# Kernel tuning notes

Hardware: AMD Instinct MI355X
Metric: run time of the kernel (lower is better)

## Reference

```python
import jax, jax.numpy as jnp
import numpy as np

N_NODES = 100000


def gcn_conv(x, edge_index, W, b):
    """PyG GCNConv: symmetric normalization with added self-loops.
    x: [N, Fin], edge_index: [2, E], W: [Fin, Fout], b: [Fout]
    """
    n = x.shape[0]
    h = x @ W  # [N, Fout] dense transform first (standard GCNConv order)
    loops = jnp.arange(n, dtype=edge_index.dtype)
    src = jnp.concatenate([edge_index[0], loops])  # self-loops appended
    dst = jnp.concatenate([edge_index[1], loops])
    deg = jax.ops.segment_sum(jnp.ones_like(dst, dtype=h.dtype), dst, num_segments=n)
    dinv = jax.lax.rsqrt(deg)  # deg >= 1 thanks to self-loops
    norm = dinv[src] * dinv[dst]  # [E+N]
    msgs = h[src] * norm[:, None]  # gather + scale
    out = jax.ops.segment_sum(msgs, dst, num_segments=n)  # scatter-add
    return out + b


def setup_inputs() -> dict:
    key = jax.random.key(0)
    k = jax.random.split(key, 9)
    in_c, hid, out_c = 128, 128, 64
    n_edges = 1600000
    x = jax.random.normal(k[0], (N_NODES, in_c), dtype=jnp.float32)
    edge_index = jax.random.randint(k[1], (2, n_edges), 0, N_NODES, dtype=jnp.int64)
    def lin(kw, kb, fan_in, fan_out):
        bound = 1.0 / np.sqrt(fan_in)
        W = jax.random.uniform(kw, (fan_in, fan_out), jnp.float32, -bound, bound)
        b = jax.random.uniform(kb, (fan_out,), jnp.float32, -bound, bound)
        return W, b
    W1, b1 = lin(k[2], k[3], in_c, hid)
    W2, b2 = lin(k[4], k[5], hid, hid)
    Wf, bf = lin(k[6], k[7], hid, out_c)
    return {"x": x, "edge_index": edge_index, "W1": W1, "b1": b1,
            "W2": W2, "b2": b2, "Wf": Wf, "bf": bf}


def reference(x, edge_index, W1, b1, W2, b2, Wf, bf):
    h = jax.nn.relu(gcn_conv(x, edge_index, W1, b1))
    h = jax.nn.relu(gcn_conv(h, edge_index, W2, b2))
    return h @ Wf + bf
```

## Files before the change

kernel.cpp:

```cpp
#include <hip/hip_runtime.h>
#include <stdint.h>

typedef short short8 __attribute__((ext_vector_type(8)));
typedef float floatx4 __attribute__((ext_vector_type(4)));
typedef float f32x2 __attribute__((ext_vector_type(2)));

#define BK 256

static __device__ __forceinline__ float bflo(unsigned int u) {
    union { unsigned int i; float f; } v; v.i = u << 16; return v.f;
}
static __device__ __forceinline__ float bfhi(unsigned int u) {
    union { unsigned int i; float f; } v; v.i = u & 0xffff0000u; return v.f;
}
static __device__ __forceinline__ unsigned short f2bf(float f) {
    union { float f; unsigned int i; } v; v.f = f;
    unsigned int u = v.i;
    unsigned int r = u + 0x7fffu + ((u >> 16) & 1u);
    return (unsigned short)(r >> 16);
}
static __device__ __forceinline__ f32x2 unp2(unsigned int u) {
    union { unsigned int i; float f; } lo, hi;
    lo.i = u << 16; hi.i = u & 0xffff0000u;
    f32x2 r; r.x = lo.f; r.y = hi.f; return r;
}


__global__ void k_zero_cnt(int* bucket_cnt, int K) {
    int i = blockIdx.x * 256 + threadIdx.x;
    if (i < K) bucket_cnt[i] = 0;
}

__global__ __launch_bounds__(256) void k_hist(const int* __restrict__ dst, int* bucket_cnt,
                                              int E, int N, int K) {
    __shared__ int h[4][512];
    int t = threadIdx.x, w = t >> 6;
    for (int i = t; i < 4 * 512; i += 256) ((int*)h)[i] = 0;
    __syncthreads();
    int per = (E + gridDim.x - 1) / gridDim.x;
    int lo = blockIdx.x * per, hi = min(lo + per, E);
    for (int e = lo + t; e < hi; e += 256) {
        unsigned int d = (unsigned int)dst[e];
        if (d < (unsigned int)N) atomicAdd(&h[w][d >> 8], 1);
    }
    __syncthreads();
    for (int i = t; i < K; i += 256) {
        int c = h[0][i] + h[1][i] + h[2][i] + h[3][i];
        if (c) atomicAdd(&bucket_cnt[i], c);
    }
}

__global__ void k_scanK(const int* __restrict__ bucket_cnt, int* bucket_off, int* bucket_cur,
                        int* row_start, int K, int N) {
    __shared__ int s[512];
    int t = threadIdx.x;
    int v = (t < K) ? bucket_cnt[t] : 0;
    s[t] = v; __syncthreads();
    for (int off = 1; off < 512; off <<= 1) {
        int x = (t >= off) ? s[t - off] : 0;
        __syncthreads();
        s[t] += x;
        __syncthreads();
    }
    if (t < K) { bucket_off[t] = s[t] - v; bucket_cur[t] = s[t] - v; }
    if (t == K - 1) { bucket_off[K] = s[t]; row_start[N] = s[t]; }
}

__global__ __launch_bounds__(256) void k_binscatter(const int* __restrict__ src,
                                                    const int* __restrict__ dst,
                                                    int* bucket_cur, unsigned int* __restrict__ tmp,
                                                    int E, int N, int K) {
    __shared__ int h[4][512];
    int t = threadIdx.x, w = t >> 6;
    for (int i = t; i < 4 * 512; i += 256) ((int*)h)[i] = 0;
    __syncthreads();
    int per = (E + gridDim.x - 1) / gridDim.x;
    int lo = blockIdx.x * per, hi = min(lo + per, E);
    for (int e = lo + t; e < hi; e += 256) {
        unsigned int d = (unsigned int)dst[e];
        if (d < (unsigned int)N) atomicAdd(&h[w][d >> 8], 1);
    }
    __syncthreads();
    for (int k = t; k < K; k += 256) {
        int c0 = h[0][k], c1 = h[1][k], c2 = h[2][k], c3 = h[3][k];
        int tot = c0 + c1 + c2 + c3;
        int base = tot ? atomicAdd(&bucket_cur[k], tot) : 0;
        h[0][k] = base; h[1][k] = base + c0; h[2][k] = base + c0 + c1;
        h[3][k] = base + c0 + c1 + c2;
    }
    __syncthreads();
    for (int e = lo + t; e < hi; e += 256) {
        unsigned int d = (unsigned int)dst[e];
        if (d < (unsigned int)N) {
            unsigned int sv = (unsigned int)src[e];
            if (sv >= (unsigned int)N) sv = 0;
            int p = atomicAdd(&h[w][d >> 8], 1);
            tmp[p] = (sv << 8) | (d & 255u);
        }
    }
}

__global__ __launch_bounds__(256) void k_fine(const unsigned int* __restrict__ tmp,
                                              const int* __restrict__ bucket_off,
                                              int* __restrict__ row_start, float* __restrict__ dinv,
                                              int* __restrict__ csr, int N) {
    __shared__ int deg4[4][BK];
    __shared__ int scn[BK];
    __shared__ int cur[BK];
    int b = blockIdx.x, t = threadIdx.x, w = t >> 6;
    int lo = bucket_off[b], hi = bucket_off[b + 1];
    for (int i = t; i < 4 * BK; i += 256) ((int*)deg4)[i] = 0;
    __syncthreads();
    for (int e = lo + t; e < hi; e += 256) atomicAdd(&deg4[w][tmp[e] & 255u], 1);
    __syncthreads();
    int v = deg4[0][t] + deg4[1][t] + deg4[2][t] + deg4[3][t];
    scn[t] = v; __syncthreads();
    for (int off = 1; off < 256; off <<= 1) {
        int x = (t >= off) ? scn[t - off] : 0;
        __syncthreads();
        scn[t] += x;
        __syncthreads();
    }
    int rs = lo + scn[t] - v;
    cur[t] = rs;
    int node = b * BK + t;
    if (node < N) { row_start[node] = rs; dinv[node] = rsqrtf((float)(v + 1)); }
    __syncthreads();
    for (int e = lo + t; e < hi; e += 256) {
        unsigned int p = tmp[e];
        int pos = atomicAdd(&cur[p & 255u], 1);
        csr[pos] = (int)(p >> 8);
    }
}


__global__ void k_wconv_all(const float* __restrict__ W1, const float* __restrict__ W2,
                            const float* __restrict__ Wf, unsigned short* __restrict__ wb1,
                            unsigned short* __restrict__ wb2, unsigned short* __restrict__ wbf) {
    int i = blockIdx.x * 256 + threadIdx.x;
    if (i < 16384) {
        int k = i >> 7, n = i & 127;
        wb1[n * 128 + k] = f2bf(W1[i]);
    } else if (i < 32768) {
        int j = i - 16384, k = j >> 7, n = j & 127;
        wb2[n * 128 + k] = f2bf(W2[j]);
    } else if (i < 40960) {
        int j = i - 32768, k = j >> 6, n = j & 63;
        wbf[n * 128 + k] = f2bf(Wf[j]);
    }
}


template <int NOUT, bool SCALE, bool BIAS, bool XF32, bool OUTF32>
__global__ __launch_bounds__(256, 2) void k_gemm(
    const void* __restrict__ Xv, const unsigned short* __restrict__ Wbf,
    const float* __restrict__ bias, const float* __restrict__ dinv,
    void* __restrict__ outv, int M, int MB) {
    __shared__ __align__(16) unsigned short Wl[NOUT * 136];
    int t = threadIdx.x;
    for (int c = t; c < NOUT * 16; c += 256) {
        short8 v = *(const short8*)(Wbf + (size_t)c * 8);
        *(short8*)(&Wl[(c >> 4) * 136 + (c & 15) * 8]) = v;
    }
    __syncthreads();

    int wave = t >> 6, lane = t & 63;
    int quad = lane >> 4, l16 = lane & 15;
    constexpr int NT = NOUT / 16;

    for (int mb = blockIdx.x; mb < MB; mb += gridDim.x) {
        int m0 = mb * 64 + wave * 16;
        int mr = m0 + l16;
        int mrc = mr < M ? mr : M - 1;

        floatx4 acc[NT];
#pragma unroll
        for (int i = 0; i < NT; i++) acc[i] = (floatx4){0.f, 0.f, 0.f, 0.f};

#pragma unroll
        for (int kc = 0; kc < 4; kc++) {
            short8 a;
            if (XF32) {
                const float* X = (const float*)Xv;
                const float* p = X + (size_t)mrc * 128 + kc * 32 + quad * 8;
                float4 xa = *(const float4*)p;
                float4 xb = *(const float4*)(p + 4);
                a[0] = (short)f2bf(xa.x); a[1] = (short)f2bf(xa.y);
                a[2] = (short)f2bf(xa.z); a[3] = (short)f2bf(xa.w);
                a[4] = (short)f2bf(xb.x); a[5] = (short)f2bf(xb.y);
                a[6] = (short)f2bf(xb.z); a[7] = (short)f2bf(xb.w);
            } else {
                const unsigned short* X = (const unsigned short*)Xv;
                a = *(const short8*)(X + (size_t)mrc * 128 + kc * 32 + quad * 8);
            }
#pragma unroll
            for (int nt = 0; nt < NT; nt++) {
                short8 b = *(const short8*)(&Wl[(nt * 16 + l16) * 136 + kc * 32 + quad * 8]);
                acc[nt] = __builtin_amdgcn_mfma_f32_16x16x32_bf16(a, b, acc[nt], 0, 0, 0);
            }
        }

#pragma unroll
        for (int i = 0; i < 4; i++) {
            int r = m0 + quad * 4 + i;
            if (r >= M) continue;
            float sc = SCALE ? dinv[r] : 1.0f;
#pragma unroll
            for (int nt = 0; nt < NT; nt++) {
                int n = nt * 16 + l16;
                float v = acc[nt][i] * sc;
                if (BIAS) v += bias[n];
                if (OUTF32) {
                    ((float*)outv)[(size_t)r * NOUT + n] = v;
                } else {
                    ((unsigned short*)outv)[(size_t)r * NOUT + n] = f2bf(v);
                }
            }
        }
    }
}


__global__ __launch_bounds__(256, 8) void k_aggregate(
    const unsigned short* __restrict__ Hs, const int* __restrict__ csr,
    const int* __restrict__ row_start,
    const float* __restrict__ dinv, const float* __restrict__ bias,
    unsigned short* __restrict__ out, int N, int E) {
    int wave = threadIdx.x >> 6, lane = threadIdx.x & 63;
    int half = lane >> 5;
    int grp = (lane >> 4) & 1;
    int c16 = lane & 15;
    int l32 = lane & 31;
    int sbase = half << 5;
    int node = blockIdx.x * 8 + wave * 2 + half;
    int Nm1 = N - 1;
    int node_c = node < N ? node : Nm1;
    unsigned int cb2 = (unsigned int)c16 << 4;
    const char* Hb = (const char*)Hs;

    int start = row_start[node_c];
    int end = row_start[node_c + 1];
    if (start < 0) start = 0;
    if (end > E) end = E;
    int cnt = end - start;
    if (cnt < 0) cnt = 0;

    uint4 us = *(const uint4*)(Hb + (((size_t)node_c << 8) | cb2));

    int pre = cnt < 32 ? cnt : 32;
    int idxv = 0;
    if (l32 < pre) idxv = min(max(csr[start + l32], 0), Nm1);

    f32x2 a01 = {0.f, 0.f}, a23 = {0.f, 0.f}, a45 = {0.f, 0.f}, a67 = {0.f, 0.f};
#define ACC8(u) do { a01 += unp2((u).x); a23 += unp2((u).y); \
                     a45 += unp2((u).z); a67 += unp2((u).w); } while (0)

    int full2 = pre >> 1;
    int it = 0;
    for (; it + 4 <= full2; it += 4) {
        int p = it * 2 + grp;
        int i0 = __shfl(idxv, sbase + p);
        int i1 = __shfl(idxv, sbase + p + 2);
        int i2 = __shfl(idxv, sbase + p + 4);
        int i3 = __shfl(idxv, sbase + p + 6);
        uint4 u0 = *(const uint4*)(Hb + (((unsigned int)i0 << 8) | cb2));
        uint4 u1 = *(const uint4*)(Hb + (((unsigned int)i1 << 8) | cb2));
        uint4 u2 = *(const uint4*)(Hb + (((unsigned int)i2 << 8) | cb2));
        uint4 u3 = *(const uint4*)(Hb + (((unsigned int)i3 << 8) | cb2));
        ACC8(u0); ACC8(u1); ACC8(u2); ACC8(u3);
    }
    for (; it < full2; it++) {
        int i0 = __shfl(idxv, sbase + it * 2 + grp);
        uint4 u0 = *(const uint4*)(Hb + (((unsigned int)i0 << 8) | cb2));
        ACC8(u0);
    }
    int eT = full2 * 2 + grp;
    int iT = __shfl(idxv, sbase + (eT < pre ? eT : 0));
    if (eT < pre) {
        uint4 u0 = *(const uint4*)(Hb + (((unsigned int)iT << 8) | cb2));
        ACC8(u0);
    }
    for (int e = start + 32 + grp; e < end; e += 2) {
        int ii = min(max(csr[e], 0), Nm1);
        uint4 u = *(const uint4*)(Hb + (((unsigned int)ii << 8) | cb2));
        ACC8(u);
    }
#undef ACC8

    float a0 = a01.x, a1 = a01.y, a2 = a23.x, a3 = a23.y;
    float a4 = a45.x, a5 = a45.y, a6 = a67.x, a7 = a67.y;

    a0 += __shfl_xor(a0, 16); a1 += __shfl_xor(a1, 16); a2 += __shfl_xor(a2, 16);
    a3 += __shfl_xor(a3, 16); a4 += __shfl_xor(a4, 16); a5 += __shfl_xor(a5, 16);
    a6 += __shfl_xor(a6, 16); a7 += __shfl_xor(a7, 16);

    a0 += bflo(us.x); a1 += bfhi(us.x); a2 += bflo(us.y); a3 += bfhi(us.y);
    a4 += bflo(us.z); a5 += bfhi(us.z); a6 += bflo(us.w); a7 += bfhi(us.w);

    float di = dinv[node_c];
    float4 b0 = *(const float4*)(bias + c16 * 8);
    float4 b1 = *(const float4*)(bias + c16 * 8 + 4);
    float r0 = fmaxf(fmaf(di, a0, b0.x), 0.f);
    float r1 = fmaxf(fmaf(di, a1, b0.y), 0.f);
    float r2 = fmaxf(fmaf(di, a2, b0.z), 0.f);
    float r3 = fmaxf(fmaf(di, a3, b0.w), 0.f);
    float r4 = fmaxf(fmaf(di, a4, b1.x), 0.f);
    float r5 = fmaxf(fmaf(di, a5, b1.y), 0.f);
    float r6 = fmaxf(fmaf(di, a6, b1.z), 0.f);
    float r7 = fmaxf(fmaf(di, a7, b1.w), 0.f);
    if (grp == 0 && node < N) {
        uint4 o;
        o.x = (unsigned int)f2bf(r0) | ((unsigned int)f2bf(r1) << 16);
        o.y = (unsigned int)f2bf(r2) | ((unsigned int)f2bf(r3) << 16);
        o.z = (unsigned int)f2bf(r4) | ((unsigned int)f2bf(r5) << 16);
        o.w = (unsigned int)f2bf(r6) | ((unsigned int)f2bf(r7) << 16);
        *(uint4*)(out + (((size_t)node << 7) | (size_t)(c16 * 8))) = o;
    }
}


extern "C" void kernel_launch(void* const* d_in, const int* in_sizes, int n_in,
                              void* d_out, int out_size, void* d_ws, size_t ws_size,
                              hipStream_t stream) {
    const float* x  = (const float*)d_in[0];
    const int* ei   = (const int*)d_in[1];
    const float* W1 = (const float*)d_in[2];
    const float* b1 = (const float*)d_in[3];
    const float* W2 = (const float*)d_in[4];
    const float* b2 = (const float*)d_in[5];
    const float* Wf = (const float*)d_in[6];
    const float* bf = (const float*)d_in[7];

    int N = in_sizes[0] / 128;
    int E = in_sizes[1] / 2;
    const int* src = ei;
    const int* dst = ei + E;
    int K = (N + BK - 1) / BK;
    if (N >= (1 << 24) || K > 512) return;

    size_t need = 0;
    auto pad = [](size_t b) { return (b + 255) & ~(size_t)255; };
    size_t o_bcnt = need; need += pad(512 * 4);
    size_t o_boff = need; need += pad(513 * 4);
    size_t o_bcur = need; need += pad(512 * 4);
    size_t o_rs   = need; need += pad(((size_t)N + 1) * 4);
    size_t o_dinv = need; need += pad((size_t)N * 4);
    size_t o_wbf  = need; need += pad((16384 + 16384 + 8192) * 2);
    size_t o_csr  = need; need += pad((size_t)E * 4);
    size_t o_hs   = need; need += pad((size_t)N * 128 * 2);
    size_t o_a    = need; need += pad((size_t)N * 128 * 2);
    if (ws_size < need) return;
    if ((size_t)E * 4 > (size_t)N * 128 * 2) return;

    char* ws = (char*)d_ws;
    int* bucket_cnt = (int*)(ws + o_bcnt);
    int* bucket_off = (int*)(ws + o_boff);
    int* bucket_cur = (int*)(ws + o_bcur);
    int* row_start  = (int*)(ws + o_rs);
    float* dinv     = (float*)(ws + o_dinv);
    unsigned short* wb1 = (unsigned short*)(ws + o_wbf);
    unsigned short* wb2 = wb1 + 16384;
    unsigned short* wbf = wb2 + 16384;
    int* csr        = (int*)(ws + o_csr);
    unsigned short* Hs = (unsigned short*)(ws + o_hs);
    unsigned short* A  = (unsigned short*)(ws + o_a);
    unsigned int* tmp  = (unsigned int*)A;

    k_wconv_all<<<160, 256, 0, stream>>>(W1, W2, Wf, wb1, wb2, wbf);

    k_zero_cnt<<<2, 256, 0, stream>>>(bucket_cnt, 512);
    k_hist<<<256, 256, 0, stream>>>(dst, bucket_cnt, E, N, K);
    k_scanK<<<1, 512, 0, stream>>>(bucket_cnt, bucket_off, bucket_cur, row_start, K, N);
    k_binscatter<<<256, 256, 0, stream>>>(src, dst, bucket_cur, tmp, E, N, K);
    k_fine<<<K, 256, 0, stream>>>(tmp, bucket_off, row_start, dinv, csr, N);

    int MB = (N + 63) / 64;
    int GG = (MB + 1) / 2;

    k_gemm<128, true, false, true, false><<<GG, 256, 0, stream>>>(x, wb1, nullptr, dinv, Hs, N, MB);
    k_aggregate<<<(N + 7) / 8, 256, 0, stream>>>(Hs, csr, row_start, dinv, b1, A, N, E);
    k_gemm<128, true, false, false, false><<<GG, 256, 0, stream>>>(A, wb2, nullptr, dinv, Hs, N, MB);
    k_aggregate<<<(N + 7) / 8, 256, 0, stream>>>(Hs, csr, row_start, dinv, b2, A, N, E);
    k_gemm<64, false, true, false, true><<<GG, 256, 0, stream>>>(A, wbf, bf, nullptr, d_out, N, MB);
}
```

Before: 327.6 us.

## Fuse CSR construction kernels into one cooperative kernel with grid syncs

Replaces the six preprocessing launches (weight conversion, counter zeroing, histogram, bucket scan, bin scatter, fine sort) with a single cooperative kernel that separates the phases with grid-wide syncs. The histogram is recomputed per block in the scatter phase so each block can reserve contiguous slots per bucket. This is meant to remove launch gaps and per-kernel tail effects. It adds grid.sync costs, requires every block to be co-resident, and falls back to the old launch sequence if the cooperative launch fails.

```diff
diff --git a/kernel.cpp b/kernel.cpp
--- a/kernel.cpp
+++ b/kernel.cpp
@@ -1,4 +1,5 @@
 #include <hip/hip_runtime.h>
+#include <hip/hip_cooperative_groups.h>
 #include <stdint.h>
 
 typedef short short8 __attribute__((ext_vector_type(8)));
@@ -23,6 +24,137 @@
     union { unsigned int i; float f; } lo, hi;
     lo.i = u << 16; hi.i = u & 0xffff0000u;
     f32x2 r; r.x = lo.f; r.y = hi.f; return r;
+}
+
+
+static __device__ void wconv_body(int i, const float* W1, const float* W2, const float* Wf,
+                                  unsigned short* wb1, unsigned short* wb2, unsigned short* wbf) {
+    if (i < 16384) {
+        int k = i >> 7, n = i & 127;
+        wb1[n * 128 + k] = f2bf(W1[i]);
+    } else if (i < 32768) {
+        int j = i - 16384, k = j >> 7, n = j & 127;
+        wb2[n * 128 + k] = f2bf(W2[j]);
+    } else if (i < 40960) {
+        int j = i - 32768, k = j >> 6, n = j & 63;
+        wbf[n * 128 + k] = f2bf(Wf[j]);
+    }
+}
+
+
+__global__ __launch_bounds__(256) void k_csr_fused(
+    const int* __restrict__ src, const int* __restrict__ dst,
+    const float* __restrict__ W1, const float* __restrict__ W2, const float* __restrict__ Wf,
+    unsigned short* __restrict__ wb1, unsigned short* __restrict__ wb2,
+    unsigned short* __restrict__ wbf,
+    int* bucket_cnt, int* bucket_off, int* bucket_cur,
+    int* __restrict__ row_start, float* __restrict__ dinv,
+    unsigned int* __restrict__ tmp, int* __restrict__ csr,
+    int E, int N, int K) {
+    cooperative_groups::grid_group grid = cooperative_groups::this_grid();
+    __shared__ int h[4][512];
+    __shared__ int s[512];
+    __shared__ int deg4[4][BK];
+    int t = threadIdx.x, w = t >> 6;
+    int G = gridDim.x;
+    int g0 = blockIdx.x * 256 + t, gs = G * 256;
+
+    for (int i = g0; i < 512; i += gs) bucket_cnt[i] = 0;
+    for (int i = g0; i < 40960; i += gs) wconv_body(i, W1, W2, Wf, wb1, wb2, wbf);
+    grid.sync();
+
+    {
+        for (int i = t; i < 4 * 512; i += 256) ((int*)h)[i] = 0;
+        __syncthreads();
+        int per = (E + G - 1) / G;
+        int lo = blockIdx.x * per, hi = min(lo + per, E);
+        for (int e = lo + t; e < hi; e += 256) {
+            unsigned int d = (unsigned int)dst[e];
+            if (d < (unsigned int)N) atomicAdd(&h[w][d >> 8], 1);
+        }
+        __syncthreads();
+        for (int i = t; i < K; i += 256) {
+            int c = h[0][i] + h[1][i] + h[2][i] + h[3][i];
+            if (c) atomicAdd(&bucket_cnt[i], c);
+        }
+    }
+    grid.sync();
+
+    if (blockIdx.x == 0) {
+        int e0 = bucket_cnt[2 * t], e1 = bucket_cnt[2 * t + 1];
+        int p = e0 + e1;
+        s[t] = p; __syncthreads();
+        for (int off = 1; off < 256; off <<= 1) {
+            int x = (t >= off) ? s[t - off] : 0;
+            __syncthreads();
+            s[t] += x;
+            __syncthreads();
+        }
+        int incl = s[t];
+        int excl = incl - p;
+        bucket_off[2 * t] = excl;        bucket_cur[2 * t] = excl;
+        bucket_off[2 * t + 1] = excl + e0; bucket_cur[2 * t + 1] = excl + e0;
+        if (t == 255) { bucket_off[512] = incl; row_start[N] = incl; }
+    }
+    grid.sync();
+
+    {
+        for (int i = t; i < 4 * 512; i += 256) ((int*)h)[i] = 0;
+        __syncthreads();
+        int per = (E + G - 1) / G;
+        int lo = blockIdx.x * per, hi = min(lo + per, E);
+        for (int e = lo + t; e < hi; e += 256) {
+            unsigned int d = (unsigned int)dst[e];
+            if (d < (unsigned int)N) atomicAdd(&h[w][d >> 8], 1);
+        }
+        __syncthreads();
+        for (int k = t; k < K; k += 256) {
+            int c0 = h[0][k], c1 = h[1][k], c2 = h[2][k], c3 = h[3][k];
+            int tot = c0 + c1 + c2 + c3;
+            int base = tot ? atomicAdd(&bucket_cur[k], tot) : 0;
+            h[0][k] = base; h[1][k] = base + c0; h[2][k] = base + c0 + c1;
+            h[3][k] = base + c0 + c1 + c2;
+        }
+        __syncthreads();
+        for (int e = lo + t; e < hi; e += 256) {
+            unsigned int d = (unsigned int)dst[e];
+            if (d < (unsigned int)N) {
+                unsigned int sv = (unsigned int)src[e];
+                if (sv >= (unsigned int)N) sv = 0;
+                int p = atomicAdd(&h[w][d >> 8], 1);
+                tmp[p] = (sv << 8) | (d & 255u);
+            }
+        }
+    }
+    grid.sync();
+
+    int* scn = s;
+    int* cur = s + 256;
+    for (int b = blockIdx.x; b < K; b += G) {
+        int lo = bucket_off[b], hi = bucket_off[b + 1];
+        for (int i = t; i < 4 * BK; i += 256) ((int*)deg4)[i] = 0;
+        __syncthreads();
+        for (int e = lo + t; e < hi; e += 256) atomicAdd(&deg4[w][tmp[e] & 255u], 1);
+        __syncthreads();
+        int v = deg4[0][t] + deg4[1][t] + deg4[2][t] + deg4[3][t];
+        scn[t] = v; __syncthreads();
+        for (int off = 1; off < 256; off <<= 1) {
+            int x = (t >= off) ? scn[t - off] : 0;
+            __syncthreads();
+            scn[t] += x;
+            __syncthreads();
+        }
+        int rs = lo + scn[t] - v;
+        cur[t] = rs;
+        int node = b * BK + t;
+        if (node < N) { row_start[node] = rs; dinv[node] = rsqrtf((float)(v + 1)); }
+        __syncthreads();
+        for (int e = lo + t; e < hi; e += 256) {
+            unsigned int p = tmp[e];
+            int pos = atomicAdd(&cur[p & 255u], 1);
+            csr[pos] = (int)(p >> 8);
+        }
+    }
 }
 
 
@@ -133,21 +265,11 @@
     }
 }
 
-
 __global__ void k_wconv_all(const float* __restrict__ W1, const float* __restrict__ W2,
                             const float* __restrict__ Wf, unsigned short* __restrict__ wb1,
                             unsigned short* __restrict__ wb2, unsigned short* __restrict__ wbf) {
     int i = blockIdx.x * 256 + threadIdx.x;
-    if (i < 16384) {
-        int k = i >> 7, n = i & 127;
-        wb1[n * 128 + k] = f2bf(W1[i]);
-    } else if (i < 32768) {
-        int j = i - 16384, k = j >> 7, n = j & 127;
-        wb2[n * 128 + k] = f2bf(W2[j]);
-    } else if (i < 40960) {
-        int j = i - 32768, k = j >> 6, n = j & 63;
-        wbf[n * 128 + k] = f2bf(Wf[j]);
-    }
+    wconv_body(i, W1, W2, Wf, wb1, wb2, wbf);
 }
 
 
@@ -366,13 +488,31 @@
     unsigned short* A  = (unsigned short*)(ws + o_a);
     unsigned int* tmp  = (unsigned int*)A;
 
-    k_wconv_all<<<160, 256, 0, stream>>>(W1, W2, Wf, wb1, wb2, wbf);
-
-    k_zero_cnt<<<2, 256, 0, stream>>>(bucket_cnt, 512);
-    k_hist<<<256, 256, 0, stream>>>(dst, bucket_cnt, E, N, K);
-    k_scanK<<<1, 512, 0, stream>>>(bucket_cnt, bucket_off, bucket_cur, row_start, K, N);
-    k_binscatter<<<256, 256, 0, stream>>>(src, dst, bucket_cur, tmp, E, N, K);
-    k_fine<<<K, 256, 0, stream>>>(tmp, bucket_off, row_start, dinv, csr, N);
+    int G = K > 256 ? K : 256;
+    {
+        const int* srcp = src; const int* dstp = dst;
+        const float *W1p = W1, *W2p = W2, *Wfp = Wf;
+        unsigned short *wb1p = wb1, *wb2p = wb2, *wbfp = wbf;
+        int Ev = E, Nv = N, Kv = K;
+        void* args[] = {
+            (void*)&srcp, (void*)&dstp,
+            (void*)&W1p, (void*)&W2p, (void*)&Wfp,
+            (void*)&wb1p, (void*)&wb2p, (void*)&wbfp,
+            (void*)&bucket_cnt, (void*)&bucket_off, (void*)&bucket_cur,
+            (void*)&row_start, (void*)&dinv,
+            (void*)&tmp, (void*)&csr,
+            (void*)&Ev, (void*)&Nv, (void*)&Kv};
+        hipError_t ce = hipLaunchCooperativeKernel((const void*)k_csr_fused,
+                                                   dim3(G), dim3(256), args, 0, stream);
+        if (ce != hipSuccess) {
+            k_wconv_all<<<160, 256, 0, stream>>>(W1, W2, Wf, wb1, wb2, wbf);
+            k_zero_cnt<<<2, 256, 0, stream>>>(bucket_cnt, 512);
+            k_hist<<<256, 256, 0, stream>>>(dst, bucket_cnt, E, N, K);
+            k_scanK<<<1, 512, 0, stream>>>(bucket_cnt, bucket_off, bucket_cur, row_start, K, N);
+            k_binscatter<<<256, 256, 0, stream>>>(src, dst, bucket_cur, tmp, E, N, K);
+            k_fine<<<K, 256, 0, stream>>>(tmp, bucket_off, row_start, dinv, csr, N);
+        }
+    }
 
     int MB = (N + 63) / 64;
     int GG = (MB + 1) / 2;
```

After: 520.0 us. 58.7% more time.

## Fuse neighbor aggregation with following GEMM via shared-memory tile

Applied to the files above, without the earlier changes.

Merges each aggregation kernel with the next dense transform. Each block aggregates 64 nodes into an LDS tile, then runs bf16 MFMA against the weights, so the intermediate activation no longer makes a round trip through global memory and two launches are removed. It also folds the bucket-counter zeroing into the weight-conversion kernel. In exchange, occupancy drops from 8 to 3 blocks per CU, and each wave handles 8 nodes serially, which reduces the latency hiding available to the irregular gathers.

```diff
diff --git a/kernel.cpp b/kernel.cpp
--- a/kernel.cpp
+++ b/kernel.cpp
@@ -26,9 +26,22 @@
 }
 
 
-__global__ void k_zero_cnt(int* bucket_cnt, int K) {
+__global__ void k_wconv_all(const float* __restrict__ W1, const float* __restrict__ W2,
+                            const float* __restrict__ Wf, unsigned short* __restrict__ wb1,
+                            unsigned short* __restrict__ wb2, unsigned short* __restrict__ wbf,
+                            int* __restrict__ bucket_cnt) {
     int i = blockIdx.x * 256 + threadIdx.x;
-    if (i < K) bucket_cnt[i] = 0;
+    if (i < 512) bucket_cnt[i] = 0;
+    if (i < 16384) {
+        int k = i >> 7, n = i & 127;
+        wb1[n * 128 + k] = f2bf(W1[i]);
+    } else if (i < 32768) {
+        int j = i - 16384, k = j >> 7, n = j & 127;
+        wb2[n * 128 + k] = f2bf(W2[j]);
+    } else if (i < 40960) {
+        int j = i - 32768, k = j >> 6, n = j & 63;
+        wbf[n * 128 + k] = f2bf(Wf[j]);
+    }
 }
 
 __global__ __launch_bounds__(256) void k_hist(const int* __restrict__ dst, int* bucket_cnt,
@@ -130,23 +143,6 @@
         unsigned int p = tmp[e];
         int pos = atomicAdd(&cur[p & 255u], 1);
         csr[pos] = (int)(p >> 8);
-    }
-}
-
-
-__global__ void k_wconv_all(const float* __restrict__ W1, const float* __restrict__ W2,
-                            const float* __restrict__ Wf, unsigned short* __restrict__ wb1,
-                            unsigned short* __restrict__ wb2, unsigned short* __restrict__ wbf) {
-    int i = blockIdx.x * 256 + threadIdx.x;
-    if (i < 16384) {
-        int k = i >> 7, n = i & 127;
-        wb1[n * 128 + k] = f2bf(W1[i]);
-    } else if (i < 32768) {
-        int j = i - 16384, k = j >> 7, n = j & 127;
-        wb2[n * 128 + k] = f2bf(W2[j]);
-    } else if (i < 40960) {
-        int j = i - 32768, k = j >> 6, n = j & 63;
-        wbf[n * 128 + k] = f2bf(Wf[j]);
     }
 }
 
@@ -221,100 +217,147 @@
 }
 
 
-__global__ __launch_bounds__(256, 8) void k_aggregate(
+template <int NOUT, bool SCALE, bool BIAS, bool OUTF32>
+__global__ __launch_bounds__(256, 3) void k_agg_gemm(
     const unsigned short* __restrict__ Hs, const int* __restrict__ csr,
-    const int* __restrict__ row_start,
-    const float* __restrict__ dinv, const float* __restrict__ bias,
-    unsigned short* __restrict__ out, int N, int E) {
-    int wave = threadIdx.x >> 6, lane = threadIdx.x & 63;
+    const int* __restrict__ row_start, const float* __restrict__ dinv,
+    const float* __restrict__ bias_agg, const unsigned short* __restrict__ Wbf,
+    const float* __restrict__ bias_out, void* __restrict__ outv,
+    int N, int E) {
+    __shared__ __align__(16) unsigned short Wl[NOUT * 136];
+    __shared__ __align__(16) unsigned short Xl[64 * 136];
+    int t = threadIdx.x;
+    for (int c = t; c < NOUT * 16; c += 256) {
+        short8 v = *(const short8*)(Wbf + (size_t)c * 8);
+        *(short8*)(&Wl[(c >> 4) * 136 + (c & 15) * 8]) = v;
+    }
+
+    int wave = t >> 6, lane = t & 63;
     int half = lane >> 5;
     int grp = (lane >> 4) & 1;
     int c16 = lane & 15;
     int l32 = lane & 31;
     int sbase = half << 5;
-    int node = blockIdx.x * 8 + wave * 2 + half;
     int Nm1 = N - 1;
-    int node_c = node < N ? node : Nm1;
     unsigned int cb2 = (unsigned int)c16 << 4;
     const char* Hb = (const char*)Hs;
 
-    int start = row_start[node_c];
-    int end = row_start[node_c + 1];
-    if (start < 0) start = 0;
-    if (end > E) end = E;
-    int cnt = end - start;
-    if (cnt < 0) cnt = 0;
-
-    uint4 us = *(const uint4*)(Hb + (((size_t)node_c << 8) | cb2));
-
-    int pre = cnt < 32 ? cnt : 32;
-    int idxv = 0;
-    if (l32 < pre) idxv = min(max(csr[start + l32], 0), Nm1);
-
-    f32x2 a01 = {0.f, 0.f}, a23 = {0.f, 0.f}, a45 = {0.f, 0.f}, a67 = {0.f, 0.f};
+    float4 bA0 = *(const float4*)(bias_agg + c16 * 8);
+    float4 bA1 = *(const float4*)(bias_agg + c16 * 8 + 4);
+
+    for (int j = 0; j < 8; ++j) {
+        int lr = wave * 16 + 2 * j + half;
+        int node = blockIdx.x * 64 + lr;
+        int node_c = node < N ? node : Nm1;
+
+        int start = row_start[node_c];
+        int end = row_start[node_c + 1];
+        if (start < 0) start = 0;
+        if (end > E) end = E;
+        int cnt = end - start;
+        if (cnt < 0) cnt = 0;
+
+        uint4 us = *(const uint4*)(Hb + (((size_t)node_c << 8) | cb2));
+
+        int pre = cnt < 32 ? cnt : 32;
+        int idxv = 0;
+        if (l32 < pre) idxv = min(max(csr[start + l32], 0), Nm1);
+
+        f32x2 a01 = {0.f, 0.f}, a23 = {0.f, 0.f}, a45 = {0.f, 0.f}, a67 = {0.f, 0.f};
 #define ACC8(u) do { a01 += unp2((u).x); a23 += unp2((u).y); \
                      a45 += unp2((u).z); a67 += unp2((u).w); } while (0)
-
-    int full2 = pre >> 1;
-    int it = 0;
-    for (; it + 4 <= full2; it += 4) {
-        int p = it * 2 + grp;
-        int i0 = __shfl(idxv, sbase + p);
-        int i1 = __shfl(idxv, sbase + p + 2);
-        int i2 = __shfl(idxv, sbase + p + 4);
-        int i3 = __shfl(idxv, sbase + p + 6);
-        uint4 u0 = *(const uint4*)(Hb + (((unsigned int)i0 << 8) | cb2));
-        uint4 u1 = *(const uint4*)(Hb + (((unsigned int)i1 << 8) | cb2));
-        uint4 u2 = *(const uint4*)(Hb + (((unsigned int)i2 << 8) | cb2));
-        uint4 u3 = *(const uint4*)(Hb + (((unsigned int)i3 << 8) | cb2));
-        ACC8(u0); ACC8(u1); ACC8(u2); ACC8(u3);
-    }
-    for (; it < full2; it++) {
-        int i0 = __shfl(idxv, sbase + it * 2 + grp);
-        uint4 u0 = *(const uint4*)(Hb + (((unsigned int)i0 << 8) | cb2));
-        ACC8(u0);
-    }
-    int eT = full2 * 2 + grp;
-    int iT = __shfl(idxv, sbase + (eT < pre ? eT : 0));
-    if (eT < pre) {
-        uint4 u0 = *(const uint4*)(Hb + (((unsigned int)iT << 8) | cb2));
-        ACC8(u0);
-    }
-    for (int e = start + 32 + grp; e < end; e += 2) {
-        int ii = min(max(csr[e], 0), Nm1);
-        uint4 u = *(const uint4*)(Hb + (((unsigned int)ii << 8) | cb2));
-        ACC8(u);
-    }
+        int full2 = pre >> 1;
+        int it = 0;
+        for (; it + 4 <= full2; it += 4) {
+            int p = it * 2 + grp;
+            int i0 = __shfl(idxv, sbase + p);
+            int i1 = __shfl(idxv, sbase + p + 2);
+            int i2 = __shfl(idxv, sbase + p + 4);
+            int i3 = __shfl(idxv, sbase + p + 6);
+            uint4 u0 = *(const uint4*)(Hb + (((unsigned int)i0 << 8) | cb2));
+            uint4 u1 = *(const uint4*)(Hb + (((unsigned int)i1 << 8) | cb2));
+            uint4 u2 = *(const uint4*)(Hb + (((unsigned int)i2 << 8) | cb2));
+            uint4 u3 = *(const uint4*)(Hb + (((unsigned int)i3 << 8) | cb2));
+            ACC8(u0); ACC8(u1); ACC8(u2); ACC8(u3);
+        }
+        for (; it < full2; it++) {
+            int i0 = __shfl(idxv, sbase + it * 2 + grp);
+            uint4 u0 = *(const uint4*)(Hb + (((unsigned int)i0 << 8) | cb2));
+            ACC8(u0);
+        }
+        int eT = full2 * 2 + grp;
+        int iT = __shfl(idxv, sbase + (eT < pre ? eT : 0));
+        if (eT < pre) {
+            uint4 u0 = *(const uint4*)(Hb + (((unsigned int)iT << 8) | cb2));
+            ACC8(u0);
+        }
+        for (int e = start + 32 + grp; e < end; e += 2) {
+            int ii = min(max(csr[e], 0), Nm1);
+            uint4 u = *(const uint4*)(Hb + (((unsigned int)ii << 8) | cb2));
+            ACC8(u);
+        }
 #undef ACC8
 
-    float a0 = a01.x, a1 = a01.y, a2 = a23.x, a3 = a23.y;
-    float a4 = a45.x, a5 = a45.y, a6 = a67.x, a7 = a67.y;
-
-    a0 += __shfl_xor(a0, 16); a1 += __shfl_xor(a1, 16); a2 += __shfl_xor(a2, 16);
-    a3 += __shfl_xor(a3, 16); a4 += __shfl_xor(a4, 16); a5 += __shfl_xor(a5, 16);
-    a6 += __shfl_xor(a6, 16); a7 += __shfl_xor(a7, 16);
-
-    a0 += bflo(us.x); a1 += bfhi(us.x); a2 += bflo(us.y); a3 += bfhi(us.y);
-    a4 += bflo(us.z); a5 += bfhi(us.z); a6 += bflo(us.w); a7 += bfhi(us.w);
-
-    float di = dinv[node_c];
-    float4 b0 = *(const float4*)(bias + c16 * 8);
-    float4 b1 = *(const float4*)(bias + c16 * 8 + 4);
-    float r0 = fmaxf(fmaf(di, a0, b0.x), 0.f);
-    float r1 = fmaxf(fmaf(di, a1, b0.y), 0.f);
-    float r2 = fmaxf(fmaf(di, a2, b0.z), 0.f);
-    float r3 = fmaxf(fmaf(di, a3, b0.w), 0.f);
-    float r4 = fmaxf(fmaf(di, a4, b1.x), 0.f);
-    float r5 = fmaxf(fmaf(di, a5, b1.y), 0.f);
-    float r6 = fmaxf(fmaf(di, a6, b1.z), 0.f);
-    float r7 = fmaxf(fmaf(di, a7, b1.w), 0.f);
-    if (grp == 0 && node < N) {
-        uint4 o;
-        o.x = (unsigned int)f2bf(r0) | ((unsigned int)f2bf(r1) << 16);
-        o.y = (unsigned int)f2bf(r2) | ((unsigned int)f2bf(r3) << 16);
-        o.z = (unsigned int)f2bf(r4) | ((unsigned int)f2bf(r5) << 16);
-        o.w = (unsigned int)f2bf(r6) | ((unsigned int)f2bf(r7) << 16);
-        *(uint4*)(out + (((size_t)node << 7) | (size_t)(c16 * 8))) = o;
+        float a0 = a01.x, a1 = a01.y, a2 = a23.x, a3 = a23.y;
+        float a4 = a45.x, a5 = a45.y, a6 = a67.x, a7 = a67.y;
+
+        a0 += __shfl_xor(a0, 16); a1 += __shfl_xor(a1, 16); a2 += __shfl_xor(a2, 16);
+        a3 += __shfl_xor(a3, 16); a4 += __shfl_xor(a4, 16); a5 += __shfl_xor(a5, 16);
+        a6 += __shfl_xor(a6, 16); a7 += __shfl_xor(a7, 16);
+
+        a0 += bflo(us.x); a1 += bfhi(us.x); a2 += bflo(us.y); a3 += bfhi(us.y);
+        a4 += bflo(us.z); a5 += bfhi(us.z); a6 += bflo(us.w); a7 += bfhi(us.w);
+
+        float di = dinv[node_c];
+        if (grp == 0) {
+            short8 o;
+            o[0] = (short)f2bf(fmaxf(fmaf(di, a0, bA0.x), 0.f));
+            o[1] = (short)f2bf(fmaxf(fmaf(di, a1, bA0.y), 0.f));
+            o[2] = (short)f2bf(fmaxf(fmaf(di, a2, bA0.z), 0.f));
+            o[3] = (short)f2bf(fmaxf(fmaf(di, a3, bA0.w), 0.f));
+            o[4] = (short)f2bf(fmaxf(fmaf(di, a4, bA1.x), 0.f));
+            o[5] = (short)f2bf(fmaxf(fmaf(di, a5, bA1.y), 0.f));
+            o[6] = (short)f2bf(fmaxf(fmaf(di, a6, bA1.z), 0.f));
+            o[7] = (short)f2bf(fmaxf(fmaf(di, a7, bA1.w), 0.f));
+            *(short8*)(&Xl[lr * 136 + c16 * 8]) = o;
+        }
+    }
+    __syncthreads();
+
+    int quad = lane >> 4, l16 = lane & 15;
+    constexpr int NT = NOUT / 16;
+    int m0 = blockIdx.x * 64 + wave * 16;
+
+    floatx4 acc[NT];
+#pragma unroll
+    for (int i = 0; i < NT; i++) acc[i] = (floatx4){0.f, 0.f, 0.f, 0.f};
+
+#pragma unroll
+    for (int kc = 0; kc < 4; kc++) {
+        short8 a = *(const short8*)(&Xl[(wave * 16 + l16) * 136 + kc * 32 + quad * 8]);
+#pragma unroll
+        for (int nt = 0; nt < NT; nt++) {
+            short8 b = *(const short8*)(&Wl[(nt * 16 + l16) * 136 + kc * 32 + quad * 8]);
+            acc[nt] = __builtin_amdgcn_mfma_f32_16x16x32_bf16(a, b, acc[nt], 0, 0, 0);
+        }
+    }
+
+#pragma unroll
+    for (int i = 0; i < 4; i++) {
+        int r = m0 + quad * 4 + i;
+        if (r >= N) continue;
+        float sc = SCALE ? dinv[r] : 1.0f;
+#pragma unroll
+        for (int nt = 0; nt < NT; nt++) {
+            int n = nt * 16 + l16;
+            float v = acc[nt][i] * sc;
+            if (BIAS) v += bias_out[n];
+            if (OUTF32) {
+                ((float*)outv)[(size_t)r * NOUT + n] = v;
+            } else {
+                ((unsigned short*)outv)[(size_t)r * NOUT + n] = f2bf(v);
+            }
+        }
     }
 }
 
@@ -362,13 +405,11 @@
     unsigned short* wb2 = wb1 + 16384;
     unsigned short* wbf = wb2 + 16384;
     int* csr        = (int*)(ws + o_csr);
-    unsigned short* Hs = (unsigned short*)(ws + o_hs);
-    unsigned short* A  = (unsigned short*)(ws + o_a);
-    unsigned int* tmp  = (unsigned int*)A;
-
-    k_wconv_all<<<160, 256, 0, stream>>>(W1, W2, Wf, wb1, wb2, wbf);
-
-    k_zero_cnt<<<2, 256, 0, stream>>>(bucket_cnt, 512);
+    unsigned short* Hs  = (unsigned short*)(ws + o_hs);
+    unsigned short* Hs2 = (unsigned short*)(ws + o_a);
+    unsigned int* tmp   = (unsigned int*)Hs2;
+
+    k_wconv_all<<<160, 256, 0, stream>>>(W1, W2, Wf, wb1, wb2, wbf, bucket_cnt);
     k_hist<<<256, 256, 0, stream>>>(dst, bucket_cnt, E, N, K);
     k_scanK<<<1, 512, 0, stream>>>(bucket_cnt, bucket_off, bucket_cur, row_start, K, N);
     k_binscatter<<<256, 256, 0, stream>>>(src, dst, bucket_cur, tmp, E, N, K);
@@ -378,8 +419,8 @@
     int GG = (MB + 1) / 2;
 
     k_gemm<128, true, false, true, false><<<GG, 256, 0, stream>>>(x, wb1, nullptr, dinv, Hs, N, MB);
-    k_aggregate<<<(N + 7) / 8, 256, 0, stream>>>(Hs, csr, row_start, dinv, b1, A, N, E);
-    k_gemm<128, true, false, false, false><<<GG, 256, 0, stream>>>(A, wb2, nullptr, dinv, Hs, N, MB);
-    k_aggregate<<<(N + 7) / 8, 256, 0, stream>>>(Hs, csr, row_start, dinv, b2, A, N, E);
-    k_gemm<64, false, true, false, true><<<GG, 256, 0, stream>>>(A, wbf, bf, nullptr, d_out, N, MB);
-}
+    k_agg_gemm<128, true, false, false><<<MB, 256, 0, stream>>>(
+        Hs, csr, row_start, dinv, b1, wb2, nullptr, Hs2, N, E);
+    k_agg_gemm<64, false, true, true><<<MB, 256, 0, stream>>>(
+        Hs2, csr, row_start, dinv, b2, wbf, bf, d_out, N, E);
+}
```

Measured after the change: 348.6 us. 6.4% more time.
